# Kernel tuning notes

Hardware: AMD Instinct MI355X
Metric: run time of the kernel (lower is better)

The kernel has to match this reference:

```python
import jax, jax.numpy as jnp
import numpy as np

DIM = 1024
NUM_HEADS = 16
HEAD_DIM = DIM // NUM_HEADS
B, S = 2, 2048


def setup_inputs() -> dict:
    key = jax.random.key(0)
    ks = jax.random.split(key, 7)
    x = jax.random.normal(ks[0], (B, S, DIM), dtype=jnp.float32)
    cos = jax.random.uniform(ks[1], (S, HEAD_DIM // 2), dtype=jnp.float32)
    sin = jax.random.uniform(ks[2], (S, HEAD_DIM // 2), dtype=jnp.float32)
    scale = 1.0 / np.sqrt(DIM)
    Wq = jax.random.normal(ks[3], (DIM, DIM), dtype=jnp.float32) * scale
    Wk = jax.random.normal(ks[4], (DIM, DIM), dtype=jnp.float32) * scale
    Wv = jax.random.normal(ks[5], (DIM, DIM), dtype=jnp.float32) * scale
    Wo = jax.random.normal(ks[6], (DIM, DIM), dtype=jnp.float32) * scale
    return {"x": x, "cos": cos, "sin": sin, "Wq": Wq, "Wk": Wk, "Wv": Wv, "Wo": Wo}


def _apply_rope(t, c, s):
    # t: [B, S, H, hd]; c, s: [1, S, 1, hd] (already doubled)
    half = t.shape[-1] // 2
    t1, t2 = t[..., :half], t[..., half:]
    rot = jnp.concatenate([-t2, t1], axis=-1)
    return t * c + rot * s


def reference(x, cos, sin, Wq, Wk, Wv, Wo):
    Bs, Ss, D = x.shape
    H, hd = NUM_HEADS, HEAD_DIM
    q = (x @ Wq).reshape(Bs, Ss, H, hd)
    k = (x @ Wk).reshape(Bs, Ss, H, hd)
    v = (x @ Wv).reshape(Bs, Ss, H, hd)
    # repeat(1,1,1,2) in torch tiles cos as [cos, cos] along last dim
    c = jnp.concatenate([cos, cos], axis=-1)[None, :, None, :]
    s = jnp.concatenate([sin, sin], axis=-1)[None, :, None, :]
    q = _apply_rope(q, c, s)
    k = _apply_rope(k, c, s)
    # SDPA, non-causal, scale 1/sqrt(hd)
    scores = jnp.einsum("bqhd,bkhd->bhqk", q, k) / jnp.sqrt(jnp.float32(hd))
    attn = jax.nn.softmax(scores, axis=-1)
    out = jnp.einsum("bhqk,bkhd->bqhd", attn, v).reshape(Bs, Ss, D)
    return out @ Wo
```

## Files before the change

### kernel.cpp

```cpp
#include <hip/hip_runtime.h>

#define B_  2
#define S_  2048
#define D_  1024
#define H_  16
#define HD_ 64
#define M_  (B_*S_)

typedef __bf16 bf16x8 __attribute__((ext_vector_type(8)));
typedef float  f32x4  __attribute__((ext_vector_type(4)));
typedef float  f32x16 __attribute__((ext_vector_type(16)));
typedef unsigned short ushort_t;

static __device__ __forceinline__ ushort_t f2bf(float f) {
  __bf16 b = (__bf16)f;
  return __builtin_bit_cast(ushort_t, b);
}
static __device__ __forceinline__ float bf2f(ushort_t u) {
  return (float)__builtin_bit_cast(__bf16, u);
}

typedef __attribute__((address_space(1))) const unsigned u32g;
typedef __attribute__((address_space(3))) unsigned u32l;
static __device__ __forceinline__ void gll16(const ushort_t* g, __bf16* l) {
  __builtin_amdgcn_global_load_lds((u32g*)g, (u32l*)l, 16, 0, 0);
}

__global__ __launch_bounds__(256) void convert_x(const float* __restrict__ x,
                                                 ushort_t* __restrict__ xb) {
  size_t e = ((size_t)blockIdx.x * 256 + threadIdx.x) * 8;
  float4 a = *(const float4*)(x + e);
  float4 b = *(const float4*)(x + e + 4);
  uint4 pk;
  pk.x = (unsigned)f2bf(a.x) | ((unsigned)f2bf(a.y) << 16);
  pk.y = (unsigned)f2bf(a.z) | ((unsigned)f2bf(a.w) << 16);
  pk.z = (unsigned)f2bf(b.x) | ((unsigned)f2bf(b.y) << 16);
  pk.w = (unsigned)f2bf(b.z) | ((unsigned)f2bf(b.w) << 16);
  *(uint4*)(xb + e) = pk;
}

__global__ __launch_bounds__(256) void transpose_w(const float* __restrict__ Wq,
                                                   const float* __restrict__ Wk,
                                                   const float* __restrict__ Wv,
                                                   const float* __restrict__ Wo,
                                                   ushort_t* __restrict__ Wqkvt,
                                                   ushort_t* __restrict__ Wot) {
  __shared__ __bf16 T[64][72];
  const int z = blockIdx.z;
  const float* W = (z == 0) ? Wq : (z == 1) ? Wk : (z == 2) ? Wv : Wo;
  ushort_t* Wt = (z < 3) ? (Wqkvt + (size_t)z * 1048576) : Wot;
  const int k0 = blockIdx.y * 64, n0 = blockIdx.x * 64;
  const int t = threadIdx.x, r = t >> 2, c16 = (t & 3) * 16;
#pragma unroll
  for (int i = 0; i < 4; i++) {
    float4 v = *(const float4*)(W + (size_t)(k0 + r) * D_ + n0 + c16 + i * 4);
    T[r][c16 + i*4 + 0] = (__bf16)v.x;
    T[r][c16 + i*4 + 1] = (__bf16)v.y;
    T[r][c16 + i*4 + 2] = (__bf16)v.z;
    T[r][c16 + i*4 + 3] = (__bf16)v.w;
  }
  __syncthreads();
  ushort_t vals[16];
#pragma unroll
  for (int i = 0; i < 16; i++) vals[i] = __builtin_bit_cast(ushort_t, T[c16 + i][r]);
  ushort_t* dst = Wt + (size_t)(n0 + r) * D_ + k0 + c16;
  *(uint4*)dst       = *(const uint4*)&vals[0];
  *(uint4*)(dst + 8) = *(const uint4*)&vals[8];
}

__global__ __launch_bounds__(256) void transpose_v(const ushort_t* __restrict__ Vb,
                                                   ushort_t* __restrict__ Vtg) {
  __shared__ __bf16 T[64][72];
  const int bh = blockIdx.y, kt = blockIdx.x;
  const int t = threadIdx.x, r = t >> 2, c16 = (t & 3) * 16;
  const ushort_t* src = Vb + ((size_t)bh * S_ + kt*64 + r) * 64 + c16;
  *(uint4*)&T[r][c16]     = *(const uint4*)src;
  *(uint4*)&T[r][c16 + 8] = *(const uint4*)(src + 8);
  __syncthreads();
  ushort_t vals[16];
#pragma unroll
  for (int i = 0; i < 16; i++) {
    int c = c16 + i;
    int k = ((c & 1) << 5) | (c >> 1);
    vals[i] = __builtin_bit_cast(ushort_t, T[k][r]);
  }
  ushort_t* dst = Vtg + ((size_t)bh * 64 + r) * S_ + kt*64 + c16;
  *(uint4*)dst       = *(const uint4*)&vals[0];
  *(uint4*)(dst + 8) = *(const uint4*)&vals[8];
}

template<int OMODE, int BN>
__global__ __launch_bounds__(256) void gemm_bf16(const ushort_t* __restrict__ A,
                                                 const ushort_t* __restrict__ Bt,
                                                 void* __restrict__ Cp,
                                                 const float* __restrict__ cosb,
                                                 const float* __restrict__ sinb) {
  constexpr int NF = BN / 32;
  __shared__ __bf16 As[4096];
  __shared__ __bf16 Bs[BN * 32];
  const int t = threadIdx.x, w = t >> 6, lane = t & 63, l15 = lane & 15, g = lane >> 4;
  const int wr = w >> 1, wc = w & 1;
  const int row0 = blockIdx.y * 128, col0 = blockIdx.x * BN;
  const int lr = t >> 2, lc = (t & 3) * 8;
  f32x4 acc[4][NF] = {};

  for (int k0 = 0; k0 < D_; k0 += 32) {
    __syncthreads();
#pragma unroll
    for (int i = 0; i < 2; i++)
      gll16(A + (size_t)(row0 + i*64 + lr) * D_ + k0 + lc, &As[i*2048 + w*512]);
#pragma unroll
    for (int i = 0; i < BN/64; i++)
      gll16(Bt + (size_t)(col0 + i*64 + lr) * D_ + k0 + lc, &Bs[i*2048 + w*512]);
    __syncthreads();
    bf16x8 af[4], bfv[NF];
#pragma unroll
    for (int mt = 0; mt < 4; mt++)  af[mt]  = *(const bf16x8*)&As[(wr*64 + mt*16 + l15)*32 + g*8];
#pragma unroll
    for (int nt = 0; nt < NF; nt++) bfv[nt] = *(const bf16x8*)&Bs[(wc*(BN/2) + nt*16 + l15)*32 + g*8];
#pragma unroll
    for (int mt = 0; mt < 4; mt++)
#pragma unroll
      for (int nt = 0; nt < NF; nt++)
        acc[mt][nt] = __builtin_amdgcn_mfma_f32_16x16x32_bf16(af[mt], bfv[nt], acc[mt][nt], 0, 0, 0);
  }

  if (OMODE == 0) {
#pragma unroll
    for (int mt = 0; mt < 4; mt++)
#pragma unroll
      for (int nt = 0; nt < NF; nt++) {
        int col = col0 + wc*(BN/2) + nt*16 + l15;
#pragma unroll
        for (int reg = 0; reg < 4; reg++) {
          int r = row0 + wr*64 + mt*16 + g*4 + reg;
          ((float*)Cp)[(size_t)r * D_ + col] = acc[mt][nt][reg];
        }
      }
  } else {
    const int mat = col0 >> 10;
    const int nc0 = (col0 + wc*64) & 1023;
    const int h = nc0 >> 6;
    ushort_t* dst = (ushort_t*)Cp + (size_t)mat * 4194304;
    const float QS = 0.125f * 1.4426950408889634f;
#pragma unroll
    for (int mt = 0; mt < 4; mt++) {
#pragma unroll
      for (int reg = 0; reg < 4; reg++) {
        int r = row0 + wr*64 + mt*16 + g*4 + reg;
        int b = r >> 11, s = r & (S_ - 1);
        size_t base = (((size_t)(b*H_ + h) * S_ + s) << 6);
        if (mat < 2) {
#pragma unroll
          for (int nt = 0; nt < 2; nt++) {
            int d1 = nt*16 + l15;
            float c  = cosb[s*32 + d1];
            float sn = sinb[s*32 + d1];
            float v1 = acc[mt][nt][reg], v2 = acc[mt][nt+2][reg];
            float r1 = v1*c - v2*sn;
            float r2 = v2*c + v1*sn;
            if (mat == 0) { r1 *= QS; r2 *= QS; }
            dst[base + d1]      = f2bf(r1);
            dst[base + d1 + 32] = f2bf(r2);
          }
        } else {
#pragma unroll
          for (int nt = 0; nt < 4; nt++)
            dst[base + nt*16 + l15] = f2bf(acc[mt][nt][reg]);
        }
      }
    }
  }
}

__global__ __launch_bounds__(256) void attn32(const ushort_t* __restrict__ Q,
                                              const ushort_t* __restrict__ K,
                                              const ushort_t* __restrict__ Vtg,
                                              ushort_t* __restrict__ op0,
                                              ushort_t* __restrict__ op1,
                                              float* __restrict__ lw) {
  __shared__ __bf16 Ks[64][72];
  __shared__ __bf16 Vt[64][72];
  __shared__ __bf16 Ps[4][32][72];
  const int t = threadIdx.x, w = t >> 6, lane = t & 63;
  const int l31 = lane & 31, h2 = lane >> 5;
  const int bh = blockIdx.y, q0 = blockIdx.x * 128 + w * 32, z = blockIdx.z;

  const ushort_t* Qp = Q + ((size_t)bh * S_ + q0 + l31) * HD_;
  bf16x8 qf[4];
#pragma unroll
  for (int kc = 0; kc < 4; kc++) qf[kc] = *(const bf16x8*)(Qp + kc*16 + h2*8);

  f32x16 o0 = {}, o1 = {};
  float lp[16];
#pragma unroll
  for (int i = 0; i < 16; i++) lp[i] = 0.f;

  const ushort_t* Kb = K   + ((size_t)bh * S_ + z * 1024) * HD_;
  const ushort_t* Vg = Vtg + (size_t)bh * HD_ * S_ + z * 1024;
  const int sr = t >> 3, sc8 = (t & 7) * 8;

  uint4 ka, kb, va, vb;
  ka = *(const uint4*)(Kb + (size_t)(sr)      * HD_ + sc8);
  kb = *(const uint4*)(Kb + (size_t)(sr + 32) * HD_ + sc8);
  va = *(const uint4*)(Vg + (size_t)(sr)      * S_  + sc8);
  vb = *(const uint4*)(Vg + (size_t)(sr + 32) * S_  + sc8);

  for (int kt = 0; kt < 16; kt++) {
    __syncthreads();
    *(uint4*)&Ks[sr][sc8]      = ka;
    *(uint4*)&Ks[sr + 32][sc8] = kb;
    *(uint4*)&Vt[sr][sc8]      = va;
    *(uint4*)&Vt[sr + 32][sc8] = vb;
    __syncthreads();
    if (kt < 15) {
      ka = *(const uint4*)(Kb + (size_t)((kt+1)*64 + sr)      * HD_ + sc8);
      kb = *(const uint4*)(Kb + (size_t)((kt+1)*64 + sr + 32) * HD_ + sc8);
      va = *(const uint4*)(Vg + (size_t)(sr)      * S_ + (kt+1)*64 + sc8);
      vb = *(const uint4*)(Vg + (size_t)(sr + 32) * S_ + (kt+1)*64 + sc8);
    }

    f32x16 s0 = {}, s1 = {};
#pragma unroll
    for (int kc = 0; kc < 4; kc++) {
      bf16x8 b0 = *(const bf16x8*)&Ks[l31][kc*16 + h2*8];
      bf16x8 b1 = *(const bf16x8*)&Ks[32 + l31][kc*16 + h2*8];
      s0 = __builtin_amdgcn_mfma_f32_32x32x16_bf16(qf[kc], b0, s0, 0, 0, 0);
      s1 = __builtin_amdgcn_mfma_f32_32x32x16_bf16(qf[kc], b1, s1, 0, 0, 0);
    }

#pragma unroll
    for (int i = 0; i < 16; i++) {
      float p0 = exp2f(s0[i]);
      float p1 = exp2f(s1[i]);
      lp[i] += p0 + p1;
      int row = (i & 3) + 8*(i >> 2) + 4*h2;
      unsigned pk = (unsigned)f2bf(p0) | ((unsigned)f2bf(p1) << 16);
      *(unsigned*)&Ps[w][row][2*l31] = pk;
    }

#pragma unroll
    for (int kc = 0; kc < 4; kc++) {
      bf16x8 pf = *(const bf16x8*)&Ps[w][l31][kc*16 + h2*8];
      bf16x8 v0 = *(const bf16x8*)&Vt[l31][kc*16 + h2*8];
      bf16x8 v1 = *(const bf16x8*)&Vt[32 + l31][kc*16 + h2*8];
      o0 = __builtin_amdgcn_mfma_f32_32x32x16_bf16(pf, v0, o0, 0, 0, 0);
      o1 = __builtin_amdgcn_mfma_f32_32x32x16_bf16(pf, v1, o1, 0, 0, 0);
    }
  }

#pragma unroll
  for (int i = 0; i < 16; i++) {
#pragma unroll
    for (int mk = 1; mk < 32; mk <<= 1) lp[i] += __shfl_xor(lp[i], mk, 64);
  }

  ushort_t* op = (z == 0) ? op0 : op1;
  float* lwp = lw + (size_t)(z*32 + bh) * S_;
#pragma unroll
  for (int i = 0; i < 16; i++) {
    int row = q0 + (i & 3) + 8*(i >> 2) + 4*h2;
    size_t base = ((size_t)bh * S_ + row) * 64;
    op[base + l31]      = f2bf(o0[i]);
    op[base + 32 + l31] = f2bf(o1[i]);
    if (l31 == 0) lwp[row] = lp[i];
  }
}

__global__ __launch_bounds__(256) void combine(const ushort_t* __restrict__ op0,
                                               const ushort_t* __restrict__ op1,
                                               const float* __restrict__ lw,
                                               ushort_t* __restrict__ att) {
  int tid = blockIdx.x * 256 + threadIdx.x;
  int d8 = (tid & 7) * 8;
  int s  = (tid >> 3) & (S_ - 1);
  int bh = tid >> 14;
  size_t pb = ((size_t)bh * S_ + s) * 64 + d8;
  uint4 a = *(const uint4*)(op0 + pb);
  uint4 b = *(const uint4*)(op1 + pb);
  float inv = 1.f / (lw[(size_t)bh * S_ + s] + lw[(size_t)(32 + bh) * S_ + s]);
  const ushort_t* as = (const ushort_t*)&a;
  const ushort_t* bs = (const ushort_t*)&b;
  ushort_t outv[8];
#pragma unroll
  for (int i = 0; i < 8; i++)
    outv[i] = f2bf((bf2f(as[i]) + bf2f(bs[i])) * inv);
  int bidx = bh >> 4, h = bh & 15;
  *(uint4*)(att + ((size_t)(bidx * S_ + s)) * D_ + h*64 + d8) = *(const uint4*)outv;
}

extern "C" void kernel_launch(void* const* d_in, const int* in_sizes, int n_in,
                              void* d_out, int out_size, void* d_ws, size_t ws_size,
                              hipStream_t stream) {
  (void)in_sizes; (void)n_in; (void)out_size; (void)ws_size;
  const float* x    = (const float*)d_in[0];
  const float* cosb = (const float*)d_in[1];
  const float* sinb = (const float*)d_in[2];
  const float* Wq   = (const float*)d_in[3];
  const float* Wk   = (const float*)d_in[4];
  const float* Wv   = (const float*)d_in[5];
  const float* Wo   = (const float*)d_in[6];
  float* out = (float*)d_out;

  ushort_t* w     = (ushort_t*)d_ws;
  ushort_t* xb    = w;
  ushort_t* Wqkvt = w + 4194304;
  ushort_t* Wot   = w + 7340032;
  ushort_t* Qb    = w + 8388608;
  ushort_t* Kb    = w + 12582912;
  ushort_t* Vb    = w + 16777216;
  ushort_t* Vtg   = w + 20971520;
  ushort_t* att   = w + 25165824;
  float*    lw    = (float*)Wqkvt;

  convert_x<<<2048, 256, 0, stream>>>(x, xb);
  transpose_w<<<dim3(16, 16, 4), 256, 0, stream>>>(Wq, Wk, Wv, Wo, Wqkvt, Wot);

  gemm_bf16<1,128><<<dim3(24, 32), 256, 0, stream>>>(xb, Wqkvt, Qb, cosb, sinb);

  transpose_v<<<dim3(32, 32), 256, 0, stream>>>(Vb, Vtg);

  attn32<<<dim3(16, 32, 2), 256, 0, stream>>>(Qb, Kb, Vtg, xb, Vb, lw);

  combine<<<2048, 256, 0, stream>>>(xb, Vb, lw, att);

  gemm_bf16<0,64><<<dim3(16, 32), 256, 0, stream>>>(att, Wot, out, nullptr, nullptr);
}
```

Measured before the change: 224.8 us.

## Load attention K/V tiles via direct global-to-LDS with XOR swizzle, 128-key tiles

Replaces register-staged K/V prefetch with direct global-to-LDS loads (gll16) into XOR-swizzled unpadded shared buffers, and doubles the key tile to 128 so each loaded tile feeds two 64-key compute phases. The aim is to drop the VGPR round trip, avoid LDS bank conflicts without padding, and halve the number of barriers per key. It also switches to the raw hardware exp2. The cost is losing the software prefetch overlap: loads are now issued and waited on between the two barriers, so latency is exposed unless other waves hide it. LDS use also grows.

```diff
diff --git a/kernel.cpp b/kernel.cpp
--- a/kernel.cpp
+++ b/kernel.cpp
@@ -179,11 +179,11 @@
                                               ushort_t* __restrict__ op0,
                                               ushort_t* __restrict__ op1,
                                               float* __restrict__ lw) {
-  __shared__ __bf16 Ks[64][72];
-  __shared__ __bf16 Vt[64][72];
+  __shared__ __bf16 KsL[128 * 64];
+  __shared__ __bf16 VtL[64 * 128];
   __shared__ __bf16 Ps[4][32][72];
   const int t = threadIdx.x, w = t >> 6, lane = t & 63;
-  const int l31 = lane & 31, h2 = lane >> 5;
+  const int l31 = lane & 31, h2 = lane >> 5, sw = l31 & 7;
   const int bh = blockIdx.y, q0 = blockIdx.x * 128 + w * 32, z = blockIdx.z;
 
   const ushort_t* Qp = Q + ((size_t)bh * S_ + q0 + l31) * HD_;
@@ -198,54 +198,60 @@
 
   const ushort_t* Kb = K   + ((size_t)bh * S_ + z * 1024) * HD_;
   const ushort_t* Vg = Vtg + (size_t)bh * HD_ * S_ + z * 1024;
-  const int sr = t >> 3, sc8 = (t & 7) * 8;
-
-  uint4 ka, kb, va, vb;
-  ka = *(const uint4*)(Kb + (size_t)(sr)      * HD_ + sc8);
-  kb = *(const uint4*)(Kb + (size_t)(sr + 32) * HD_ + sc8);
-  va = *(const uint4*)(Vg + (size_t)(sr)      * S_  + sc8);
-  vb = *(const uint4*)(Vg + (size_t)(sr + 32) * S_  + sc8);
-
-  for (int kt = 0; kt < 16; kt++) {
+
+  const int krl = lane >> 3;
+  const int kco = ((lane & 7) ^ krl) * 8;
+  const int vrl = lane >> 4;
+
+  for (int kt = 0; kt < 8; kt++) {
     __syncthreads();
-    *(uint4*)&Ks[sr][sc8]      = ka;
-    *(uint4*)&Ks[sr + 32][sc8] = kb;
-    *(uint4*)&Vt[sr][sc8]      = va;
-    *(uint4*)&Vt[sr + 32][sc8] = vb;
+#pragma unroll
+    for (int p = 0; p < 4; p++) {
+      int bk = w*8 + p*32;
+      gll16(Kb + (size_t)(kt*128 + bk + krl) * HD_ + kco, &KsL[(bk)*64]);
+    }
+#pragma unroll
+    for (int p = 0; p < 4; p++) {
+      int bd = w*4 + p*16;
+      int d  = bd + vrl;
+      int cd = (lane & 8) | ((lane & 7) ^ (d & 7));
+      gll16(Vg + (size_t)d * S_ + kt*128 + cd*8, &VtL[(bd)*128]);
+    }
     __syncthreads();
-    if (kt < 15) {
-      ka = *(const uint4*)(Kb + (size_t)((kt+1)*64 + sr)      * HD_ + sc8);
-      kb = *(const uint4*)(Kb + (size_t)((kt+1)*64 + sr + 32) * HD_ + sc8);
-      va = *(const uint4*)(Vg + (size_t)(sr)      * S_ + (kt+1)*64 + sc8);
-      vb = *(const uint4*)(Vg + (size_t)(sr + 32) * S_ + (kt+1)*64 + sc8);
-    }
-
-    f32x16 s0 = {}, s1 = {};
-#pragma unroll
-    for (int kc = 0; kc < 4; kc++) {
-      bf16x8 b0 = *(const bf16x8*)&Ks[l31][kc*16 + h2*8];
-      bf16x8 b1 = *(const bf16x8*)&Ks[32 + l31][kc*16 + h2*8];
-      s0 = __builtin_amdgcn_mfma_f32_32x32x16_bf16(qf[kc], b0, s0, 0, 0, 0);
-      s1 = __builtin_amdgcn_mfma_f32_32x32x16_bf16(qf[kc], b1, s1, 0, 0, 0);
-    }
-
-#pragma unroll
-    for (int i = 0; i < 16; i++) {
-      float p0 = exp2f(s0[i]);
-      float p1 = exp2f(s1[i]);
-      lp[i] += p0 + p1;
-      int row = (i & 3) + 8*(i >> 2) + 4*h2;
-      unsigned pk = (unsigned)f2bf(p0) | ((unsigned)f2bf(p1) << 16);
-      *(unsigned*)&Ps[w][row][2*l31] = pk;
-    }
-
-#pragma unroll
-    for (int kc = 0; kc < 4; kc++) {
-      bf16x8 pf = *(const bf16x8*)&Ps[w][l31][kc*16 + h2*8];
-      bf16x8 v0 = *(const bf16x8*)&Vt[l31][kc*16 + h2*8];
-      bf16x8 v1 = *(const bf16x8*)&Vt[32 + l31][kc*16 + h2*8];
-      o0 = __builtin_amdgcn_mfma_f32_32x32x16_bf16(pf, v0, o0, 0, 0, 0);
-      o1 = __builtin_amdgcn_mfma_f32_32x32x16_bf16(pf, v1, o1, 0, 0, 0);
+
+#pragma unroll
+    for (int ph = 0; ph < 2; ph++) {
+      f32x16 s0 = {}, s1 = {};
+#pragma unroll
+      for (int kc = 0; kc < 4; kc++) {
+        int c = kc*2 + h2;
+        int cs = (c ^ sw) * 8;
+        bf16x8 b0 = *(const bf16x8*)&KsL[(ph*64 + l31)*64      + cs];
+        bf16x8 b1 = *(const bf16x8*)&KsL[(ph*64 + 32 + l31)*64 + cs];
+        s0 = __builtin_amdgcn_mfma_f32_32x32x16_bf16(qf[kc], b0, s0, 0, 0, 0);
+        s1 = __builtin_amdgcn_mfma_f32_32x32x16_bf16(qf[kc], b1, s1, 0, 0, 0);
+      }
+
+#pragma unroll
+      for (int i = 0; i < 16; i++) {
+        float p0 = __builtin_amdgcn_exp2f(s0[i]);
+        float p1 = __builtin_amdgcn_exp2f(s1[i]);
+        lp[i] += p0 + p1;
+        int row = (i & 3) + 8*(i >> 2) + 4*h2;
+        unsigned pk = (unsigned)f2bf(p0) | ((unsigned)f2bf(p1) << 16);
+        *(unsigned*)&Ps[w][row][2*l31] = pk;
+      }
+
+#pragma unroll
+      for (int kc = 0; kc < 4; kc++) {
+        int c = kc*2 + h2;
+        int cs = (ph*8 | (c ^ sw)) * 8;
+        bf16x8 pf = *(const bf16x8*)&Ps[w][l31][kc*16 + h2*8];
+        bf16x8 v0 = *(const bf16x8*)&VtL[(l31)*128      + cs];
+        bf16x8 v1 = *(const bf16x8*)&VtL[(32 + l31)*128 + cs];
+        o0 = __builtin_amdgcn_mfma_f32_32x32x16_bf16(pf, v0, o0, 0, 0, 0);
+        o1 = __builtin_amdgcn_mfma_f32_32x32x16_bf16(pf, v1, o1, 0, 0, 0);
+      }
     }
   }
 
```

Measured after the change: 214.5 us. 4.6% less time.
